# Kernel optimization log

Hardware: AMD Instinct MI355X
Metric: run time of the kernel (lower is better)

Reference implementation:

```python
import jax, jax.numpy as jnp
import numpy as np

N_NODES = 50000
N_EDGES = 1600000
IN_DIM, HID_DIM, OUT_DIM = 512, 128, 16


def spmm(edge_src, edge_dst, edge_vals, x):
    # sparse.mm(A, x): out[dst] += A[dst, src] * x[src]
    msgs = edge_vals[:, None] * x[edge_src]  # [E, D]
    return jax.ops.segment_sum(msgs, edge_dst, num_segments=N_NODES)


def setup_inputs() -> dict:
    key = jax.random.key(0)
    k1, k2, k3, k4, k5, k6 = jax.random.split(key, 6)
    feature = jax.random.normal(k1, (N_NODES, IN_DIM), dtype=jnp.float32)
    edge_src = jax.random.randint(k2, (N_EDGES,), 0, N_NODES, dtype=jnp.int32)
    edge_dst = jax.random.randint(k3, (N_EDGES,), 0, N_NODES, dtype=jnp.int32)
    edge_vals = jax.random.uniform(k4, (N_EDGES,), dtype=jnp.float32)
    # kaiming_uniform-style init: bound = sqrt(6 / fan_in) (a=sqrt(5) omitted for simplicity of scale)
    b1 = float(np.sqrt(6.0 / IN_DIM))
    b2 = float(np.sqrt(6.0 / HID_DIM))
    W1 = jax.random.uniform(k5, (IN_DIM, HID_DIM), dtype=jnp.float32, minval=-b1, maxval=b1)
    W2 = jax.random.uniform(k6, (HID_DIM, OUT_DIM), dtype=jnp.float32, minval=-b2, maxval=b2)
    return {"feature": feature, "edge_src": edge_src, "edge_dst": edge_dst,
            "edge_vals": edge_vals, "W1": W1, "W2": W2}


def reference(feature, edge_src, edge_dst, edge_vals, W1, W2):
    # layer 1: dense matmul -> sparse aggregation -> ReLU
    h = jax.nn.relu(spmm(edge_src, edge_dst, edge_vals, feature @ W1))
    # layer 2
    out = spmm(edge_src, edge_dst, edge_vals, h @ W2)
    return out
```

## Files before the change

### kernel.cpp

```cpp
#include <hip/hip_runtime.h>

#define N_NODES 50000
#define N_EDGES 1600000
#define IN_DIM 512
#define HID_DIM 128
#define OUT_DIM 16

#define BKT_SHIFT 6
#define BKT_NODES 64
#define NB ((N_NODES + BKT_NODES - 1) / BKT_NODES)

typedef __attribute__((ext_vector_type(8))) __bf16 bf16x8;
typedef __attribute__((ext_vector_type(8))) unsigned short ushort8;
typedef __attribute__((ext_vector_type(4))) unsigned short ushort4v;
typedef __attribute__((ext_vector_type(4))) float f32x4;

static __device__ __forceinline__ unsigned short f2bf(float x) {
    unsigned int u = __float_as_uint(x);
    u += 0x7FFFu + ((u >> 16) & 1u);
    return (unsigned short)(u >> 16);
}
static __device__ __forceinline__ float bf2f(unsigned short v) {
    return __uint_as_float(((unsigned int)v) << 16);
}

__device__ inline int wave_incl_scan(int v) {
    #pragma unroll
    for (int off = 1; off < 64; off <<= 1) {
        int x = __shfl_up(v, off, 64);
        if ((threadIdx.x & 63) >= off) v += x;
    }
    return v;
}


__global__ void zero_bcnt_kernel(int* __restrict__ bcnt) {
    int t = threadIdx.x;
    if (t < NB) bcnt[t] = 0;
}

__global__ __launch_bounds__(1024) void bucket_hist_kernel(const int* __restrict__ dst,
                                                           int* __restrict__ bcnt) {
    __shared__ int lc[NB];
    const int t = threadIdx.x;
    for (int b = t; b < NB; b += 1024) lc[b] = 0;
    __syncthreads();
    const int e0 = blockIdx.x * 4096;
    #pragma unroll
    for (int i = 0; i < 4; i++) {
        int e = e0 + i * 1024 + t;
        if (e < N_EDGES) atomicAdd(&lc[dst[e] >> BKT_SHIFT], 1);
    }
    __syncthreads();
    for (int b = t; b < NB; b += 1024)
        if (lc[b]) atomicAdd(&bcnt[b], lc[b]);
}

__global__ __launch_bounds__(1024) void bucket_scan_kernel(const int* __restrict__ bcnt,
                                                           int* __restrict__ bucket_ptr,
                                                           int* __restrict__ cursor) {
    __shared__ int wsums[16];
    const int t = threadIdx.x;
    const int lane = t & 63, wid = t >> 6;
    int v = (t < NB) ? bcnt[t] : 0;
    int incl = wave_incl_scan(v);
    if (lane == 63) wsums[wid] = incl;
    __syncthreads();
    if (wid == 0) {
        int wv = (lane < 16) ? wsums[lane] : 0;
        int ws = wave_incl_scan(wv);
        if (lane < 16) wsums[lane] = ws;
    }
    __syncthreads();
    int woff = wid ? wsums[wid - 1] : 0;
    int excl = woff + incl - v;
    if (t < NB) { bucket_ptr[t] = excl; cursor[t] = excl; }
    if (t == NB - 1) bucket_ptr[NB] = excl + v;
}

__global__ __launch_bounds__(1024) void bucket_scatter_kernel(const int* __restrict__ src,
                                                              const int* __restrict__ dst,
                                                              const float* __restrict__ val,
                                                              int* __restrict__ cursor,
                                                              int2* __restrict__ pairs_bkt) {
    __shared__ int cnt[NB];
    __shared__ int bbase[NB];
    const int t = threadIdx.x;
    const int e0 = blockIdx.x * 4096;
    for (int b = t; b < NB; b += 1024) cnt[b] = 0;
    __syncthreads();
    #pragma unroll
    for (int i = 0; i < 4; i++) {
        int e = e0 + i * 1024 + t;
        if (e < N_EDGES) atomicAdd(&cnt[dst[e] >> BKT_SHIFT], 1);
    }
    __syncthreads();
    for (int b = t; b < NB; b += 1024) {
        int c = cnt[b];
        bbase[b] = c ? atomicAdd(&cursor[b], c) : 0;
        cnt[b] = 0;
    }
    __syncthreads();
    #pragma unroll
    for (int i = 0; i < 4; i++) {
        int e = e0 + i * 1024 + t;
        if (e < N_EDGES) {
            int dd = dst[e];
            int b = dd >> BKT_SHIFT, dl = dd & (BKT_NODES - 1);
            int pos = bbase[b] + atomicAdd(&cnt[b], 1);
            int2 pr;
            pr.x = src[e] | (dl << 16);
            pr.y = __float_as_int(val[e]);
            pairs_bkt[pos] = pr;
        }
    }
}

__global__ __launch_bounds__(512) void node_sort_fused_kernel(const int2* __restrict__ pairs_bkt,
                                                              const int* __restrict__ bucket_ptr,
                                                              int* __restrict__ row_ptr,
                                                              int2* __restrict__ pairs) {
    __shared__ int cnt[BKT_NODES];
    __shared__ int base[BKT_NODES];
    const int t = threadIdx.x;
    const int b = blockIdx.x;
    const int s = bucket_ptr[b], e = bucket_ptr[b + 1];
    if (t < BKT_NODES) cnt[t] = 0;
    __syncthreads();
    for (int i = s + t; i < e; i += 512)
        atomicAdd(&cnt[pairs_bkt[i].x >> 16], 1);
    __syncthreads();
    if (t < BKT_NODES) {
        int v = cnt[t];
        int incl = wave_incl_scan(v);
        base[t] = s + incl - v;
    }
    __syncthreads();
    if (t < BKT_NODES) {
        int n = b * BKT_NODES + t;
        if (n < N_NODES) row_ptr[n] = base[t];
        cnt[t] = 0;
    }
    if (b == NB - 1 && t == 0) row_ptr[N_NODES] = N_EDGES;
    __syncthreads();
    for (int i = s + t; i < e; i += 512) {
        int2 pr = pairs_bkt[i];
        int dl = pr.x >> 16;
        int p = base[dl] + atomicAdd(&cnt[dl], 1);
        pairs[p] = pr;
    }
}


__global__ void prep_w1_kernel(const float* __restrict__ W1, unsigned short* __restrict__ Wt) {
    int i = blockIdx.x * 256 + threadIdx.x;
    if (i < IN_DIM * HID_DIM) {
        int k = i >> 7, col = i & 127;
        Wt[(size_t)col * IN_DIM + k] = f2bf(W1[i]);
    }
}

#define G1_XSTR 72
#define G1_BSTR 72
__global__ __launch_bounds__(256) void gemm1_kernel(const float* __restrict__ X,
                                                    const unsigned short* __restrict__ Wt,
                                                    unsigned short* __restrict__ h0) {
    __shared__ __align__(16) unsigned short Xs[64 * G1_XSTR];
    __shared__ __align__(16) unsigned short Bs[128 * G1_BSTR];
    const int t = threadIdx.x;
    const int lane = t & 63;
    const int wave = t >> 6;
    const int c = lane & 15, g = lane >> 4;
    const int m0 = blockIdx.x * 64;

    f32x4 acc[4][2];
    #pragma unroll
    for (int mt = 0; mt < 4; mt++)
        #pragma unroll
        for (int nt = 0; nt < 2; nt++) acc[mt][nt] = (f32x4){0.f, 0.f, 0.f, 0.f};

    float4 xr[4];
    ushort8 br[4];

    #define G1_LOAD(kt)                                                                  \
        _Pragma("unroll")                                                                \
        for (int p = 0; p < 4; p++) {                                                    \
            int idx = p * 256 + t;                                                       \
            int xrow = idx >> 4, xseg = idx & 15;                                        \
            int grow = m0 + xrow; grow = (grow < N_NODES) ? grow : (N_NODES - 1);        \
            xr[p] = *(const float4*)&X[(size_t)grow * IN_DIM + (kt) * 64 + xseg * 4];    \
            int bcol = idx >> 3, bseg = idx & 7;                                         \
            br[p] = *(const ushort8*)&Wt[(size_t)bcol * IN_DIM + (kt) * 64 + bseg * 8];  \
        }

    G1_LOAD(0)
    for (int kt = 0; kt < 8; kt++) {
        #pragma unroll
        for (int p = 0; p < 4; p++) {
            int idx = p * 256 + t;
            int xrow = idx >> 4, xseg = idx & 15;
            ushort4v xw;
            xw[0] = f2bf(xr[p].x); xw[1] = f2bf(xr[p].y);
            xw[2] = f2bf(xr[p].z); xw[3] = f2bf(xr[p].w);
            *(ushort4v*)&Xs[xrow * G1_XSTR + xseg * 4] = xw;
            int bcol = idx >> 3, bseg = idx & 7;
            *(ushort8*)&Bs[bcol * G1_BSTR + bseg * 8] = br[p];
        }
        __syncthreads();
        if (kt < 7) G1_LOAD(kt + 1)
        #pragma unroll
        for (int ks = 0; ks < 2; ks++) {
            bf16x8 bf[2];
            #pragma unroll
            for (int nt = 0; nt < 2; nt++) {
                int col = wave * 32 + nt * 16 + c;
                bf[nt] = *(const bf16x8*)&Bs[col * G1_BSTR + ks * 32 + g * 8];
            }
            #pragma unroll
            for (int mt = 0; mt < 4; mt++) {
                bf16x8 af = *(const bf16x8*)&Xs[(mt * 16 + c) * G1_XSTR + ks * 32 + g * 8];
                #pragma unroll
                for (int nt = 0; nt < 2; nt++)
                    acc[mt][nt] = __builtin_amdgcn_mfma_f32_16x16x32_bf16(af, bf[nt],
                                                                          acc[mt][nt], 0, 0, 0);
            }
        }
        __syncthreads();
    }
    #undef G1_LOAD

    #pragma unroll
    for (int mt = 0; mt < 4; mt++) {
        #pragma unroll
        for (int r = 0; r < 4; r++) {
            int row = m0 + mt * 16 + g * 4 + r;
            if (row < N_NODES) {
                #pragma unroll
                for (int nt = 0; nt < 2; nt++) {
                    int col = wave * 32 + nt * 16 + c;
                    h0[(size_t)row * HID_DIM + col] = f2bf(acc[mt][nt][r]);
                }
            }
        }
    }
}

__global__ __launch_bounds__(256) void spmm1_node_kernel(const unsigned short* __restrict__ h0,
                                                         const int* __restrict__ row_ptr,
                                                         const int2* __restrict__ pairs,
                                                         unsigned short* __restrict__ h) {
    const int wid = __builtin_amdgcn_readfirstlane(threadIdx.x >> 6);
    const int n = blockIdx.x * 4 + wid;
    const int lane = threadIdx.x & 63;
    const int s = row_ptr[n], e = row_ptr[n + 1];
    const unsigned short* h0l = h0 + lane * 2;
    float ax = 0.f, ay = 0.f;
    for (int base = s; base < e; base += 8) {
        float vv[8];
        const unsigned short* rp[8];
        #pragma unroll
        for (int k = 0; k < 8; k++) {
            int idx = base + k;
            int cidx = (idx < e) ? idx : (e - 1);
            int2 pr = pairs[cidx];
            vv[k] = (idx < e) ? __int_as_float(pr.y) : 0.f;
            rp[k] = h0l + (size_t)(pr.x & 0xFFFF) * HID_DIM;
        }
        unsigned int gg[8];
        #pragma unroll
        for (int k = 0; k < 8; k++) gg[k] = *(const unsigned int*)rp[k];
        #pragma unroll
        for (int k = 0; k < 8; k++) {
            ax += vv[k] * bf2f((unsigned short)gg[k]);
            ay += vv[k] * bf2f((unsigned short)(gg[k] >> 16));
        }
    }
    unsigned int w = ((unsigned int)f2bf(fmaxf(ay, 0.f)) << 16) | f2bf(fmaxf(ax, 0.f));
    ((unsigned int*)(h + (size_t)n * HID_DIM))[lane] = w;
}

__global__ __launch_bounds__(256) void gemm2_kernel(const unsigned short* __restrict__ H,
                                                    const float* __restrict__ W2,
                                                    float* __restrict__ C) {
    __shared__ float Hs[16][132];
    __shared__ float Ws[128][16];
    const int t = threadIdx.x;
    const int n0 = blockIdx.x * 16;
    #pragma unroll
    for (int p = 0; p < 2; p++) {
        int idx = p * 256 + t;
        ((float4*)Ws)[idx] = ((const float4*)W2)[idx];
    }
    {
        int row = t >> 4, seg = t & 15;
        int gr = n0 + row;
        ushort8 hv = {0, 0, 0, 0, 0, 0, 0, 0};
        if (gr < N_NODES) hv = *(const ushort8*)&H[(size_t)gr * HID_DIM + seg * 8];
        #pragma unroll
        for (int j = 0; j < 8; j++) Hs[row][seg * 8 + j] = bf2f(hv[j]);
    }
    __syncthreads();
    const int nl = t >> 4, j = t & 15;
    float acc = 0.f;
    #pragma unroll 8
    for (int k = 0; k < 128; k++) acc += Hs[nl][k] * Ws[k][j];
    int n = n0 + nl;
    if (n < N_NODES) C[(size_t)n * OUT_DIM + j] = acc;
}

__global__ __launch_bounds__(256) void spmm2_node_kernel(const float* __restrict__ h2,
                                                         const int* __restrict__ row_ptr,
                                                         const int2* __restrict__ pairs,
                                                         float* __restrict__ out) {
    const int idx = blockIdx.x * 256 + threadIdx.x;
    const int n = idx >> 4;
    const int d = idx & 15;
    if (n >= N_NODES) return;
    const int s = row_ptr[n], e = row_ptr[n + 1];
    float acc = 0.f;
    int i = s;
    for (; i + 4 <= e; i += 4) {
        int2 p0 = pairs[i], p1 = pairs[i + 1], p2 = pairs[i + 2], p3 = pairs[i + 3];
        float g0 = h2[(size_t)(p0.x & 0xFFFF) * OUT_DIM + d];
        float g1 = h2[(size_t)(p1.x & 0xFFFF) * OUT_DIM + d];
        float g2 = h2[(size_t)(p2.x & 0xFFFF) * OUT_DIM + d];
        float g3 = h2[(size_t)(p3.x & 0xFFFF) * OUT_DIM + d];
        acc += __int_as_float(p0.y) * g0 + __int_as_float(p1.y) * g1
             + __int_as_float(p2.y) * g2 + __int_as_float(p3.y) * g3;
    }
    for (; i < e; i++) {
        int2 pr = pairs[i];
        acc += __int_as_float(pr.y) * h2[(size_t)(pr.x & 0xFFFF) * OUT_DIM + d];
    }
    out[(size_t)n * OUT_DIM + d] = acc;
}


extern "C" void kernel_launch(void* const* d_in, const int* in_sizes, int n_in,
                              void* d_out, int out_size, void* d_ws, size_t ws_size,
                              hipStream_t stream) {
    const float* feature   = (const float*)d_in[0];
    const int*   edge_src  = (const int*)d_in[1];
    const int*   edge_dst  = (const int*)d_in[2];
    const float* edge_vals = (const float*)d_in[3];
    const float* W1        = (const float*)d_in[4];
    const float* W2        = (const float*)d_in[5];
    float* out = (float*)d_out;

    char* ws = (char*)d_ws;
    size_t off = 0;
    auto alloc = [&](size_t bytes) {
        void* p = ws + off;
        off += (bytes + 255) & ~(size_t)255;
        return p;
    };
    unsigned short* h0    = (unsigned short*)alloc((size_t)N_NODES * HID_DIM * 2);
    unsigned short* Wt    = (unsigned short*)alloc((size_t)IN_DIM * HID_DIM * 2);
    unsigned short* h     = (unsigned short*)alloc((size_t)N_NODES * HID_DIM * 2);
    float* h2             = (float*)alloc((size_t)N_NODES * OUT_DIM * 4);
    int*   bcnt           = (int*)alloc((size_t)NB * 4);
    int*   bucket_ptr     = (int*)alloc((size_t)(NB + 1) * 4);
    int*   cursor         = (int*)alloc((size_t)NB * 4);
    int*   row_ptr        = (int*)alloc((size_t)(N_NODES + 1) * 4);
    int2*  pairs_bkt      = (int2*)alloc((size_t)N_EDGES * 8);
    int2*  pairs          = (int2*)alloc((size_t)N_EDGES * 8);

    zero_bcnt_kernel<<<1, 1024, 0, stream>>>(bcnt);
    bucket_hist_kernel<<<(N_EDGES + 4095) / 4096, 1024, 0, stream>>>(edge_dst, bcnt);
    bucket_scan_kernel<<<1, 1024, 0, stream>>>(bcnt, bucket_ptr, cursor);
    bucket_scatter_kernel<<<(N_EDGES + 4095) / 4096, 1024, 0, stream>>>(edge_src, edge_dst,
                                                                        edge_vals, cursor,
                                                                        pairs_bkt);
    node_sort_fused_kernel<<<NB, 512, 0, stream>>>(pairs_bkt, bucket_ptr, row_ptr, pairs);

    prep_w1_kernel<<<(IN_DIM * HID_DIM + 255) / 256, 256, 0, stream>>>(W1, Wt);
    gemm1_kernel<<<(N_NODES + 63) / 64, 256, 0, stream>>>(feature, Wt, h0);
    spmm1_node_kernel<<<(N_NODES + 3) / 4, 256, 0, stream>>>(h0, row_ptr, pairs, h);
    gemm2_kernel<<<(N_NODES + 15) / 16, 256, 0, stream>>>(h, W2, h2);
    spmm2_node_kernel<<<(N_NODES * 16 + 255) / 256, 256, 0, stream>>>(h2, row_ptr, pairs, out);
}
```

Before: 162.2 us.

## Precompute scatter bases, store h2 in bf16, and widen spmm2 per node

The bucket histogram now records per-block counts, and a new scan kernel turns them into per-block base offsets. The scatter kernel therefore skips its recount and its global atomics on the cursor. h2 is stored as bf16, which halves the gather traffic in the second spmm. spmm2 now uses one wave per node, with four edge groups combined by a cross-lane reduction, and gemm1 uses the native bf16 conversion. The costs are an extra kernel launch, a per-block histogram buffer, and lower precision in the second-layer messages.

After: 170.1 us. 1.05x slower.

```diff
diff --git a/kernel.cpp b/kernel.cpp
--- a/kernel.cpp
+++ b/kernel.cpp
@@ -9,10 +9,11 @@
 #define BKT_SHIFT 6
 #define BKT_NODES 64
 #define NB ((N_NODES + BKT_NODES - 1) / BKT_NODES)
+#define SC_BLOCKS ((N_EDGES + 4095) / 4096)
 
 typedef __attribute__((ext_vector_type(8))) __bf16 bf16x8;
+typedef __attribute__((ext_vector_type(4))) __bf16 bf16x4;
 typedef __attribute__((ext_vector_type(8))) unsigned short ushort8;
-typedef __attribute__((ext_vector_type(4))) unsigned short ushort4v;
 typedef __attribute__((ext_vector_type(4))) float f32x4;
 
 static __device__ __forceinline__ unsigned short f2bf(float x) {
@@ -40,7 +41,8 @@
 }
 
 __global__ __launch_bounds__(1024) void bucket_hist_kernel(const int* __restrict__ dst,
-                                                           int* __restrict__ bcnt) {
+                                                           int* __restrict__ bcnt,
+                                                           int* __restrict__ blk_hist) {
     __shared__ int lc[NB];
     const int t = threadIdx.x;
     for (int b = t; b < NB; b += 1024) lc[b] = 0;
@@ -52,13 +54,15 @@
         if (e < N_EDGES) atomicAdd(&lc[dst[e] >> BKT_SHIFT], 1);
     }
     __syncthreads();
-    for (int b = t; b < NB; b += 1024)
-        if (lc[b]) atomicAdd(&bcnt[b], lc[b]);
+    for (int b = t; b < NB; b += 1024) {
+        int c = lc[b];
+        blk_hist[(size_t)blockIdx.x * NB + b] = c;
+        if (c) atomicAdd(&bcnt[b], c);
+    }
 }
 
 __global__ __launch_bounds__(1024) void bucket_scan_kernel(const int* __restrict__ bcnt,
-                                                           int* __restrict__ bucket_ptr,
-                                                           int* __restrict__ cursor) {
+                                                           int* __restrict__ bucket_ptr) {
     __shared__ int wsums[16];
     const int t = threadIdx.x;
     const int lane = t & 63, wid = t >> 6;
@@ -74,32 +78,35 @@
     __syncthreads();
     int woff = wid ? wsums[wid - 1] : 0;
     int excl = woff + incl - v;
-    if (t < NB) { bucket_ptr[t] = excl; cursor[t] = excl; }
+    if (t < NB) bucket_ptr[t] = excl;
     if (t == NB - 1) bucket_ptr[NB] = excl + v;
+}
+
+__global__ __launch_bounds__(512) void base_scan_kernel(const int* __restrict__ bucket_ptr,
+                                                        int* __restrict__ blk_hist) {
+    const int lane = threadIdx.x & 63;
+    const int bucket = blockIdx.x * 8 + (threadIdx.x >> 6);
+    if (bucket >= NB) return;
+    int carry = bucket_ptr[bucket];
+    #pragma unroll
+    for (int c = 0; c < (SC_BLOCKS + 63) / 64; c++) {
+        int idx = c * 64 + lane;
+        int v = (idx < SC_BLOCKS) ? blk_hist[(size_t)idx * NB + bucket] : 0;
+        int incl = wave_incl_scan(v);
+        if (idx < SC_BLOCKS) blk_hist[(size_t)idx * NB + bucket] = carry + incl - v;
+        carry += __shfl(incl, 63, 64);
+    }
 }
 
 __global__ __launch_bounds__(1024) void bucket_scatter_kernel(const int* __restrict__ src,
                                                               const int* __restrict__ dst,
                                                               const float* __restrict__ val,
-                                                              int* __restrict__ cursor,
+                                                              const int* __restrict__ blk_hist,
                                                               int2* __restrict__ pairs_bkt) {
-    __shared__ int cnt[NB];
-    __shared__ int bbase[NB];
+    __shared__ int cbase[NB];
     const int t = threadIdx.x;
     const int e0 = blockIdx.x * 4096;
-    for (int b = t; b < NB; b += 1024) cnt[b] = 0;
-    __syncthreads();
-    #pragma unroll
-    for (int i = 0; i < 4; i++) {
-        int e = e0 + i * 1024 + t;
-        if (e < N_EDGES) atomicAdd(&cnt[dst[e] >> BKT_SHIFT], 1);
-    }
-    __syncthreads();
-    for (int b = t; b < NB; b += 1024) {
-        int c = cnt[b];
-        bbase[b] = c ? atomicAdd(&cursor[b], c) : 0;
-        cnt[b] = 0;
-    }
+    for (int b = t; b < NB; b += 1024) cbase[b] = blk_hist[(size_t)blockIdx.x * NB + b];
     __syncthreads();
     #pragma unroll
     for (int i = 0; i < 4; i++) {
@@ -107,7 +114,7 @@
         if (e < N_EDGES) {
             int dd = dst[e];
             int b = dd >> BKT_SHIFT, dl = dd & (BKT_NODES - 1);
-            int pos = bbase[b] + atomicAdd(&cnt[b], 1);
+            int pos = atomicAdd(&cbase[b], 1);
             int2 pr;
             pr.x = src[e] | (dl << 16);
             pr.y = __float_as_int(val[e]);
@@ -199,10 +206,10 @@
         for (int p = 0; p < 4; p++) {
             int idx = p * 256 + t;
             int xrow = idx >> 4, xseg = idx & 15;
-            ushort4v xw;
-            xw[0] = f2bf(xr[p].x); xw[1] = f2bf(xr[p].y);
-            xw[2] = f2bf(xr[p].z); xw[3] = f2bf(xr[p].w);
-            *(ushort4v*)&Xs[xrow * G1_XSTR + xseg * 4] = xw;
+            bf16x4 xw;
+            xw[0] = (__bf16)xr[p].x; xw[1] = (__bf16)xr[p].y;
+            xw[2] = (__bf16)xr[p].z; xw[3] = (__bf16)xr[p].w;
+            *(bf16x4*)&Xs[xrow * G1_XSTR + xseg * 4] = xw;
             int bcol = idx >> 3, bseg = idx & 7;
             *(ushort8*)&Bs[bcol * G1_BSTR + bseg * 8] = br[p];
         }
@@ -281,7 +288,7 @@
 
 __global__ __launch_bounds__(256) void gemm2_kernel(const unsigned short* __restrict__ H,
                                                     const float* __restrict__ W2,
-                                                    float* __restrict__ C) {
+                                                    unsigned short* __restrict__ C) {
     __shared__ float Hs[16][132];
     __shared__ float Ws[128][16];
     const int t = threadIdx.x;
@@ -305,34 +312,34 @@
     #pragma unroll 8
     for (int k = 0; k < 128; k++) acc += Hs[nl][k] * Ws[k][j];
     int n = n0 + nl;
-    if (n < N_NODES) C[(size_t)n * OUT_DIM + j] = acc;
-}
-
-__global__ __launch_bounds__(256) void spmm2_node_kernel(const float* __restrict__ h2,
+    if (n < N_NODES) C[(size_t)n * OUT_DIM + j] = f2bf(acc);
+}
+
+__global__ __launch_bounds__(256) void spmm2_node_kernel(const unsigned short* __restrict__ h2,
                                                          const int* __restrict__ row_ptr,
                                                          const int2* __restrict__ pairs,
                                                          float* __restrict__ out) {
-    const int idx = blockIdx.x * 256 + threadIdx.x;
-    const int n = idx >> 4;
-    const int d = idx & 15;
-    if (n >= N_NODES) return;
+    const int wid = __builtin_amdgcn_readfirstlane(threadIdx.x >> 6);
+    const int n = blockIdx.x * 4 + wid;
+    const int lane = threadIdx.x & 63;
+    const int g = lane >> 4, d = lane & 15;
     const int s = row_ptr[n], e = row_ptr[n + 1];
     float acc = 0.f;
-    int i = s;
-    for (; i + 4 <= e; i += 4) {
-        int2 p0 = pairs[i], p1 = pairs[i + 1], p2 = pairs[i + 2], p3 = pairs[i + 3];
-        float g0 = h2[(size_t)(p0.x & 0xFFFF) * OUT_DIM + d];
-        float g1 = h2[(size_t)(p1.x & 0xFFFF) * OUT_DIM + d];
-        float g2 = h2[(size_t)(p2.x & 0xFFFF) * OUT_DIM + d];
-        float g3 = h2[(size_t)(p3.x & 0xFFFF) * OUT_DIM + d];
-        acc += __int_as_float(p0.y) * g0 + __int_as_float(p1.y) * g1
-             + __int_as_float(p2.y) * g2 + __int_as_float(p3.y) * g3;
-    }
-    for (; i < e; i++) {
-        int2 pr = pairs[i];
-        acc += __int_as_float(pr.y) * h2[(size_t)(pr.x & 0xFFFF) * OUT_DIM + d];
-    }
-    out[(size_t)n * OUT_DIM + d] = acc;
+    for (int base = s; base < e; base += 8) {
+        int i0 = base + g, i1 = base + 4 + g;
+        int c0 = (i0 < e) ? i0 : (e - 1);
+        int c1 = (i1 < e) ? i1 : (e - 1);
+        int2 p0 = pairs[c0];
+        int2 p1 = pairs[c1];
+        float v0 = (i0 < e) ? __int_as_float(p0.y) : 0.f;
+        float v1 = (i1 < e) ? __int_as_float(p1.y) : 0.f;
+        unsigned short g0 = h2[(size_t)(p0.x & 0xFFFF) * OUT_DIM + d];
+        unsigned short g1 = h2[(size_t)(p1.x & 0xFFFF) * OUT_DIM + d];
+        acc += v0 * bf2f(g0) + v1 * bf2f(g1);
+    }
+    acc += __shfl_xor(acc, 16, 64);
+    acc += __shfl_xor(acc, 32, 64);
+    if (lane < 16) out[(size_t)n * OUT_DIM + lane] = acc;
 }
 
 
@@ -357,25 +364,25 @@
     unsigned short* h0    = (unsigned short*)alloc((size_t)N_NODES * HID_DIM * 2);
     unsigned short* Wt    = (unsigned short*)alloc((size_t)IN_DIM * HID_DIM * 2);
     unsigned short* h     = (unsigned short*)alloc((size_t)N_NODES * HID_DIM * 2);
-    float* h2             = (float*)alloc((size_t)N_NODES * OUT_DIM * 4);
+    unsigned short* h2    = (unsigned short*)alloc((size_t)N_NODES * OUT_DIM * 2);
     int*   bcnt           = (int*)alloc((size_t)NB * 4);
     int*   bucket_ptr     = (int*)alloc((size_t)(NB + 1) * 4);
-    int*   cursor         = (int*)alloc((size_t)NB * 4);
+    int*   blk_hist       = (int*)alloc((size_t)SC_BLOCKS * NB * 4);
     int*   row_ptr        = (int*)alloc((size_t)(N_NODES + 1) * 4);
     int2*  pairs_bkt      = (int2*)alloc((size_t)N_EDGES * 8);
     int2*  pairs          = (int2*)alloc((size_t)N_EDGES * 8);
 
     zero_bcnt_kernel<<<1, 1024, 0, stream>>>(bcnt);
-    bucket_hist_kernel<<<(N_EDGES + 4095) / 4096, 1024, 0, stream>>>(edge_dst, bcnt);
-    bucket_scan_kernel<<<1, 1024, 0, stream>>>(bcnt, bucket_ptr, cursor);
-    bucket_scatter_kernel<<<(N_EDGES + 4095) / 4096, 1024, 0, stream>>>(edge_src, edge_dst,
-                                                                        edge_vals, cursor,
-                                                                        pairs_bkt);
+    bucket_hist_kernel<<<SC_BLOCKS, 1024, 0, stream>>>(edge_dst, bcnt, blk_hist);
+    bucket_scan_kernel<<<1, 1024, 0, stream>>>(bcnt, bucket_ptr);
+    base_scan_kernel<<<(NB + 7) / 8, 512, 0, stream>>>(bucket_ptr, blk_hist);
+    bucket_scatter_kernel<<<SC_BLOCKS, 1024, 0, stream>>>(edge_src, edge_dst, edge_vals,
+                                                          blk_hist, pairs_bkt);
     node_sort_fused_kernel<<<NB, 512, 0, stream>>>(pairs_bkt, bucket_ptr, row_ptr, pairs);
 
     prep_w1_kernel<<<(IN_DIM * HID_DIM + 255) / 256, 256, 0, stream>>>(W1, Wt);
     gemm1_kernel<<<(N_NODES + 63) / 64, 256, 0, stream>>>(feature, Wt, h0);
     spmm1_node_kernel<<<(N_NODES + 3) / 4, 256, 0, stream>>>(h0, row_ptr, pairs, h);
     gemm2_kernel<<<(N_NODES + 15) / 16, 256, 0, stream>>>(h, W2, h2);
-    spmm2_node_kernel<<<(N_NODES * 16 + 255) / 256, 256, 0, stream>>>(h2, row_ptr, pairs, out);
-}
+    spmm2_node_kernel<<<(N_NODES + 3) / 4, 256, 0, stream>>>(h2, row_ptr, pairs, out);
+}
```
